# Kernel optimization log

Measured on AMD Instinct MI355X. Metric: run time of the kernel, lower is better.

## Reference

```python
import jax, jax.numpy as jnp
import numpy as np

EPS = 1e-12  # matches torch.nn.functional.normalize default eps


def _normalize(v):
    # L2 normalize along last dim, clamping the norm like torch F.normalize
    n = jnp.linalg.norm(v, axis=-1, keepdims=True)
    return v / jnp.maximum(n, EPS)


def setup_inputs() -> dict:
    key = jax.random.key(0)
    k1, k2 = jax.random.split(key)
    B, K, D, H, W = 64, 5, 1024, 32, 32
    cue = jax.random.normal(k1, (B, K, D), dtype=jnp.float32)
    patches = jax.random.normal(k2, (B, H, W, D), dtype=jnp.float32)
    return {"cue": cue, "patches": patches}


def reference(cue, patches):
    b, k, d = cue.shape
    _, h, w, _ = patches.shape
    cue_n = _normalize(cue)
    patches_n = _normalize(patches)
    flat = patches_n.reshape(b, h * w, d)
    # cosine similarity between each cue and every patch
    sims = jnp.einsum('bkd,bnd->bkn', cue_n, flat)  # (b, k, h*w)
    idx = jnp.argmax(sims, axis=-1)                 # (b, k)
    y = idx // w + 1                                # +1 for pad offset
    x = idx % w + 1
    # zero-pad spatial dims by 1 on each side
    pad = jnp.pad(patches, ((0, 0), (1, 1), (1, 1), (0, 0)))
    offs = jnp.arange(-1, 2)
    yy = y[:, :, None, None] + offs[None, None, :, None]  # (b, k, 3, 1)
    xx = x[:, :, None, None] + offs[None, None, None, :]  # (b, k, 1, 3)
    bidx = jnp.arange(b)[:, None, None, None]
    gathered = pad[bidx, yy, xx, :]                 # (b, k, 3, 3, d)
    roi = gathered.mean(axis=(2, 3))                # (b, k, d)
    return roi
```

## Files before the change

kernel.cpp:

```cpp
#include <hip/hip_runtime.h>
#include <math.h>

#define B 64
#define K 5
#define D 1024
#define H 32
#define W 32
#define N (H * W)

__device__ __forceinline__ float wave_sum(float v) {
#pragma unroll
    for (int off = 32; off > 0; off >>= 1) v += __shfl_down(v, off, 64);
    return v;
}

__device__ __forceinline__ float dot4(float4 a, float4 b) {
    return a.x * b.x + a.y * b.y + a.z * b.z + a.w * b.w;
}

__global__ __launch_bounds__(256) void normalize_cue(const float* __restrict__ cue,
                                                     float* __restrict__ cue_n) {
    const int row = blockIdx.x;
    const int tid = threadIdx.x;
    const float4* src = (const float4*)(cue + (size_t)row * D);
    float4 p = src[tid];
    float ss = p.x * p.x + p.y * p.y + p.z * p.z + p.w * p.w;
    ss = wave_sum(ss);
    __shared__ float smem[4];
    __shared__ float s_inv;
    const int lane = tid & 63, wid = tid >> 6;
    if (lane == 0) smem[wid] = ss;
    __syncthreads();
    if (tid == 0) {
        float t = smem[0] + smem[1] + smem[2] + smem[3];
        s_inv = 1.0f / fmaxf(sqrtf(t), 1e-12f);
    }
    __syncthreads();
    const float inv = s_inv;
    float4 o = make_float4(p.x * inv, p.y * inv, p.z * inv, p.w * inv);
    ((float4*)(cue_n + (size_t)row * D))[tid] = o;
}

__global__ __launch_bounds__(256) void sims_kernel(const float* __restrict__ patches,
                                                   const float* __restrict__ cue_n,
                                                   float* __restrict__ sims) {
    const int wave = threadIdx.x >> 6;
    const int lane = threadIdx.x & 63;
    const int bn0 = blockIdx.x * 16 + wave * 4;
    const int b = bn0 >> 10;
    const int n0 = bn0 & (N - 1);

    const float4* prow = (const float4*)(patches + (size_t)bn0 * D);
    const float4* crow = (const float4*)(cue_n + (size_t)b * K * D);

    float acc[24];
#pragma unroll
    for (int v = 0; v < 24; ++v) acc[v] = 0.f;

#pragma unroll
    for (int j = 0; j < 4; ++j) {
        const int idx = j * 64 + lane;
        float4 p[4];
#pragma unroll
        for (int r = 0; r < 4; ++r) p[r] = prow[r * 256 + idx];
#pragma unroll
        for (int r = 0; r < 4; ++r) acc[r * 6] += dot4(p[r], p[r]);
#pragma unroll
        for (int k = 0; k < K; ++k) {
            float4 c = crow[k * 256 + idx];
#pragma unroll
            for (int r = 0; r < 4; ++r) acc[r * 6 + 1 + k] += dot4(p[r], c);
        }
    }

#pragma unroll
    for (int i = 0; i < 12; ++i) {
        float t = (lane & 1) ? acc[i] : acc[i + 12];
        float r = __shfl_xor(t, 1, 64);
        acc[i] = ((lane & 1) ? acc[i + 12] : acc[i]) + r;
    }
#pragma unroll
    for (int i = 0; i < 6; ++i) {
        float t = (lane & 2) ? acc[i] : acc[i + 6];
        float r = __shfl_xor(t, 2, 64);
        acc[i] = ((lane & 2) ? acc[i + 6] : acc[i]) + r;
    }
#pragma unroll
    for (int i = 0; i < 3; ++i) {
        float t = (lane & 4) ? acc[i] : acc[i + 3];
        float r = __shfl_xor(t, 4, 64);
        acc[i] = ((lane & 4) ? acc[i + 3] : acc[i]) + r;
    }
#pragma unroll
    for (int m = 8; m <= 32; m <<= 1) {
#pragma unroll
        for (int i = 0; i < 3; ++i) acc[i] += __shfl_xor(acc[i], m, 64);
    }

    __shared__ float slab[4][24];
    if (lane < 8) {
        const int base = 12 * (lane & 1) + 6 * ((lane >> 1) & 1) + 3 * ((lane >> 2) & 1);
        slab[wave][base + 0] = acc[0];
        slab[wave][base + 1] = acc[1];
        slab[wave][base + 2] = acc[2];
    }
    __syncthreads();
    if (lane < 4 * K) {
        const int r = lane / K, k = lane % K;
        const float inv = 1.0f / fmaxf(sqrtf(slab[wave][r * 6]), 1e-12f);
        sims[((size_t)b * K + k) * N + n0 + r] = slab[wave][r * 6 + 1 + k] * inv;
    }
}

__global__ __launch_bounds__(256) void argmax_gather(const float* __restrict__ sims,
                                                     const float* __restrict__ patches,
                                                     float* __restrict__ out) {
    const int row = blockIdx.x;
    const int b = row / K;
    const int tid = threadIdx.x;

    const float4* srow = (const float4*)(sims + (size_t)row * N);
    float4 v = srow[tid];
    float best = v.x;
    int bidx = tid * 4;
    if (v.y > best) { best = v.y; bidx = tid * 4 + 1; }
    if (v.z > best) { best = v.z; bidx = tid * 4 + 2; }
    if (v.w > best) { best = v.w; bidx = tid * 4 + 3; }
#pragma unroll
    for (int off = 32; off > 0; off >>= 1) {
        const float ov = __shfl_down(best, off, 64);
        const int oi = __shfl_down(bidx, off, 64);
        if (ov > best || (ov == best && oi < bidx)) { best = ov; bidx = oi; }
    }
    __shared__ float sv[4];
    __shared__ int si[4];
    __shared__ int s_final;
    const int lane = tid & 63, wid = tid >> 6;
    if (lane == 0) { sv[wid] = best; si[wid] = bidx; }
    __syncthreads();
    if (tid == 0) {
        float bv = sv[0];
        int bi = si[0];
        for (int w2 = 1; w2 < 4; ++w2) {
            if (sv[w2] > bv || (sv[w2] == bv && si[w2] < bi)) { bv = sv[w2]; bi = si[w2]; }
        }
        s_final = bi;
    }
    __syncthreads();

    const int idx = s_final;
    const int y0 = idx >> 5;
    const int x0 = idx & 31;

    float4 acc = make_float4(0.f, 0.f, 0.f, 0.f);
#pragma unroll
    for (int dy = -1; dy <= 1; ++dy) {
        const int yy = y0 + dy;
        if (yy < 0 || yy >= H) continue;
#pragma unroll
        for (int dx = -1; dx <= 1; ++dx) {
            const int xx = x0 + dx;
            if (xx < 0 || xx >= W) continue;
            const float4* nrow =
                (const float4*)(patches + (((size_t)b * H + yy) * W + xx) * D);
            float4 p = nrow[tid];
            acc.x += p.x; acc.y += p.y; acc.z += p.z; acc.w += p.w;
        }
    }
    const float inv9 = 1.0f / 9.0f;
    float4 o = make_float4(acc.x * inv9, acc.y * inv9, acc.z * inv9, acc.w * inv9);
    ((float4*)(out + (size_t)row * D))[tid] = o;
}

extern "C" void kernel_launch(void* const* d_in, const int* in_sizes, int n_in,
                              void* d_out, int out_size, void* d_ws, size_t ws_size,
                              hipStream_t stream) {
    const float* cue = (const float*)d_in[0];
    const float* patches = (const float*)d_in[1];
    float* out = (float*)d_out;

    float* cue_n = (float*)d_ws;
    float* sims = cue_n + (size_t)B * K * D;

    normalize_cue<<<B * K, 256, 0, stream>>>(cue, cue_n);
    sims_kernel<<<(B * N) / 16, 256, 0, stream>>>(patches, cue_n, sims);
    argmax_gather<<<B * K, 256, 0, stream>>>(sims, patches, out);
}
```

Baseline: 362.8 us.

## Fuse argmax into similarity kernel via packed 64-bit atomicMax and drop cue normalization

```diff
diff --git a/kernel.cpp b/kernel.cpp
--- a/kernel.cpp
+++ b/kernel.cpp
@@ -8,42 +8,16 @@
 #define W 32
 #define N (H * W)
 
-__device__ __forceinline__ float wave_sum(float v) {
-#pragma unroll
-    for (int off = 32; off > 0; off >>= 1) v += __shfl_down(v, off, 64);
-    return v;
-}
+typedef unsigned long long u64;
+typedef unsigned int u32;
 
 __device__ __forceinline__ float dot4(float4 a, float4 b) {
     return a.x * b.x + a.y * b.y + a.z * b.z + a.w * b.w;
 }
 
-__global__ __launch_bounds__(256) void normalize_cue(const float* __restrict__ cue,
-                                                     float* __restrict__ cue_n) {
-    const int row = blockIdx.x;
-    const int tid = threadIdx.x;
-    const float4* src = (const float4*)(cue + (size_t)row * D);
-    float4 p = src[tid];
-    float ss = p.x * p.x + p.y * p.y + p.z * p.z + p.w * p.w;
-    ss = wave_sum(ss);
-    __shared__ float smem[4];
-    __shared__ float s_inv;
-    const int lane = tid & 63, wid = tid >> 6;
-    if (lane == 0) smem[wid] = ss;
-    __syncthreads();
-    if (tid == 0) {
-        float t = smem[0] + smem[1] + smem[2] + smem[3];
-        s_inv = 1.0f / fmaxf(sqrtf(t), 1e-12f);
-    }
-    __syncthreads();
-    const float inv = s_inv;
-    float4 o = make_float4(p.x * inv, p.y * inv, p.z * inv, p.w * inv);
-    ((float4*)(cue_n + (size_t)row * D))[tid] = o;
-}
-
-__global__ __launch_bounds__(256) void sims_kernel(const float* __restrict__ patches,
-                                                   const float* __restrict__ cue_n,
-                                                   float* __restrict__ sims) {
+__global__ __launch_bounds__(256) void sims_argmax(const float* __restrict__ patches,
+                                                   const float* __restrict__ cue,
+                                                   u64* __restrict__ slots) {
     const int wave = threadIdx.x >> 6;
     const int lane = threadIdx.x & 63;
     const int bn0 = blockIdx.x * 16 + wave * 4;
@@ -51,7 +25,7 @@
     const int n0 = bn0 & (N - 1);
 
     const float4* prow = (const float4*)(patches + (size_t)bn0 * D);
-    const float4* crow = (const float4*)(cue_n + (size_t)b * K * D);
+    const float4* crow = (const float4*)(cue + (size_t)b * K * D);
 
     float acc[24];
 #pragma unroll
@@ -98,6 +72,7 @@
     }
 
     __shared__ float slab[4][24];
+    __shared__ u64 cand[4][20];
     if (lane < 8) {
         const int base = 12 * (lane & 1) + 6 * ((lane >> 1) & 1) + 3 * ((lane >> 2) & 1);
         slab[wave][base + 0] = acc[0];
@@ -108,47 +83,36 @@
     if (lane < 4 * K) {
         const int r = lane / K, k = lane % K;
         const float inv = 1.0f / fmaxf(sqrtf(slab[wave][r * 6]), 1e-12f);
-        sims[((size_t)b * K + k) * N + n0 + r] = slab[wave][r * 6 + 1 + k] * inv;
+        const float s = slab[wave][r * 6 + 1 + k] * inv;
+        const u32 bits = __float_as_uint(s);
+        const u32 u = bits ^ ((bits & 0x80000000u) ? 0xFFFFFFFFu : 0x80000000u);
+        const int n = n0 + r;
+        cand[wave][lane] = ((u64)u << 32) | (u32)(N - 1 - n);
+    }
+    __syncthreads();
+    if (threadIdx.x < K) {
+        const int k = threadIdx.x;
+        u64 best = 0;
+#pragma unroll
+        for (int w2 = 0; w2 < 4; ++w2)
+#pragma unroll
+            for (int r = 0; r < 4; ++r) {
+                const u64 c = cand[w2][r * K + k];
+                if (c > best) best = c;
+            }
+        atomicMax(&slots[(size_t)b * K + k], best);
     }
 }
 
-__global__ __launch_bounds__(256) void argmax_gather(const float* __restrict__ sims,
+__global__ __launch_bounds__(256) void gather_kernel(const u64* __restrict__ slots,
                                                      const float* __restrict__ patches,
                                                      float* __restrict__ out) {
     const int row = blockIdx.x;
     const int b = row / K;
     const int tid = threadIdx.x;
 
-    const float4* srow = (const float4*)(sims + (size_t)row * N);
-    float4 v = srow[tid];
-    float best = v.x;
-    int bidx = tid * 4;
-    if (v.y > best) { best = v.y; bidx = tid * 4 + 1; }
-    if (v.z > best) { best = v.z; bidx = tid * 4 + 2; }
-    if (v.w > best) { best = v.w; bidx = tid * 4 + 3; }
-#pragma unroll
-    for (int off = 32; off > 0; off >>= 1) {
-        const float ov = __shfl_down(best, off, 64);
-        const int oi = __shfl_down(bidx, off, 64);
-        if (ov > best || (ov == best && oi < bidx)) { best = ov; bidx = oi; }
-    }
-    __shared__ float sv[4];
-    __shared__ int si[4];
-    __shared__ int s_final;
-    const int lane = tid & 63, wid = tid >> 6;
-    if (lane == 0) { sv[wid] = best; si[wid] = bidx; }
-    __syncthreads();
-    if (tid == 0) {
-        float bv = sv[0];
-        int bi = si[0];
-        for (int w2 = 1; w2 < 4; ++w2) {
-            if (sv[w2] > bv || (sv[w2] == bv && si[w2] < bi)) { bv = sv[w2]; bi = si[w2]; }
-        }
-        s_final = bi;
-    }
-    __syncthreads();
-
-    const int idx = s_final;
+    const u64 c = slots[row];
+    const int idx = (N - 1) - (int)(c & 0xFFFFFFFFull);
     const int y0 = idx >> 5;
     const int x0 = idx & 31;
 
@@ -179,10 +143,9 @@
     const float* patches = (const float*)d_in[1];
     float* out = (float*)d_out;
 
-    float* cue_n = (float*)d_ws;
-    float* sims = cue_n + (size_t)B * K * D;
+    u64* slots = (u64*)d_ws;
 
-    normalize_cue<<<B * K, 256, 0, stream>>>(cue, cue_n);
-    sims_kernel<<<(B * N) / 16, 256, 0, stream>>>(patches, cue_n, sims);
-    argmax_gather<<<B * K, 256, 0, stream>>>(sims, patches, out);
+    hipMemsetAsync(slots, 0, (size_t)B * K * sizeof(u64), stream);
+    sims_argmax<<<(B * N) / 16, 256, 0, stream>>>(patches, cue, slots);
+    gather_kernel<<<B * K, 256, 0, stream>>>(slots, patches, out);
 }
```

Measured after the change: 361.5 us. Within noise of the previous version (-0.4%).
